# Optimization experiments

Measured on AMD Instinct MI355X. Metric: run time of the kernel, lower is better.

Reference implementation:

```python
import jax, jax.numpy as jnp
import numpy as np
from jax import lax

B, V, E = 8, 1024, 32          # batch, nodes, raw node-embedding dim
F, H = 64, 4                   # node_encoding, num_heads
HID = 64                       # encoder/decoder hidden size
LAYERS = 2                     # graph_layers
FLOW_ITERS = 10
BIG = 1e9
COST_C = 1.0                   # quadratic cost: c*x^2, inv_derivative(y)=y/(2c)
DEG_P = 16.0 / V               # ~16 avg out-degree


def setup_inputs() -> dict:
    key = jax.random.key(0)
    ks = jax.random.split(key, 24)
    demands = jax.random.normal(ks[0], (B, V, 1), jnp.float32)
    demands = demands - jnp.mean(demands, axis=1, keepdims=True)  # balanced supply/demand
    node_embeddings = jax.random.normal(ks[1], (V, E), jnp.float32)
    adj = (jax.random.uniform(ks[2], (V, V)) < DEG_P).astype(jnp.float32)
    adj = jnp.maximum(adj, jnp.eye(V, dtype=jnp.float32))  # ensure nonempty rows
    s = 0.05
    p = lambda k, shp: jax.random.normal(k, shp, jnp.float32) * s
    return {
        'demands': demands, 'node_embeddings': node_embeddings, 'adj': adj,
        'enc_w1': p(ks[3], (E + 1, HID)), 'enc_b1': jnp.zeros((HID,), jnp.float32),
        'enc_w2': p(ks[4], (HID, F)),     'enc_b2': jnp.zeros((F,), jnp.float32),
        'gat_w':  p(ks[5], (H, F, F)),
        'gat_a1': p(ks[6], (H, F)), 'gat_a2': p(ks[7], (H, F)),
        'gate_w': p(ks[8], (F, F)), 'gate_u': p(ks[9], (F, F)),
        'gate_b': jnp.zeros((F,), jnp.float32),
        'dec_w1': p(ks[10], (F, HID)), 'dec_b1': jnp.zeros((HID,), jnp.float32),
        'dec_w2': p(ks[11], (HID, V)), 'dec_b2': jnp.zeros((V,), jnp.float32),
        'dual_w1': p(ks[12], (F, HID)), 'dual_b1': jnp.zeros((HID,), jnp.float32),
        'dual_w2': p(ks[13], (HID, 1)), 'dual_b2': jnp.zeros((1,), jnp.float32),
    }


def _forward(demands, node_embeddings, adj,
             enc_w1, enc_b1, enc_w2, enc_b2,
             gat_w, gat_a1, gat_a2,
             gate_w, gate_u, gate_b,
             dec_w1, dec_b1, dec_w2, dec_b2,
             dual_w1, dual_b1, dual_w2, dual_b2):
    node_bias = -BIG * (1.0 - adj)                     # [V, V]
    # ---- encoder MLP (relu hidden) ----
    x = jnp.broadcast_to(node_embeddings[None], (B, V, E))
    x = jnp.concatenate([x, demands], axis=2)          # [B, V, E+1]
    enc = jax.nn.relu(x @ enc_w1 + enc_b1) @ enc_w2 + enc_b2   # [B, V, F]
    enc = jax.nn.relu(enc)
    # ---- GAT + gate, shared weights across graph_layers ----
    for _ in range(LAYERS):
        t = jnp.einsum('bvf,hfg->bhvg', enc, gat_w)            # [B, H, V, F]
        s_self = jnp.einsum('bhvg,hg->bhv', t, gat_a1)
        s_nbr = jnp.einsum('bhvg,hg->bhv', t, gat_a2)
        logits = jax.nn.leaky_relu(s_self[..., :, None] + s_nbr[..., None, :], 0.2)
        coefs = jax.nn.softmax(logits + node_bias[None, None], axis=-1)  # [B,H,V,V]
        heads = jnp.einsum('bhvw,bhwg->bhvg', coefs, t)
        nxt = jax.nn.relu(jnp.mean(heads, axis=1))             # [B, V, F]
        z = jax.nn.sigmoid(nxt @ gate_w + enc @ gate_u + gate_b)
        enc = z * nxt + (1.0 - z) * enc
    # ---- decoder -> masked softmax flow weights ----
    pred = (enc @ dec_w1 + dec_b1) @ dec_w2 + dec_b2           # [B, V, V] (linear MLP)
    pred = jnp.square(pred)
    flow_weights = jax.nn.softmax(pred + node_bias[None], axis=-1)
    # ---- iterative min-cost-flow solve ----
    def flow_step(flow, _):
        inflow = jnp.sum(flow, axis=1)[:, :, None]             # [B, V, 1]
        return flow_weights * jax.nn.relu(inflow - demands), None
    flow, _ = lax.scan(flow_step, jnp.zeros_like(flow_weights), None, length=FLOW_ITERS)[0], None
    flow = lax.scan(flow_step, jnp.zeros_like(flow_weights), None, length=FLOW_ITERS)[0]
    flow_cost = jnp.sum(COST_C * jnp.square(flow), axis=(1, 2))  # [B]
    # ---- dual variables / dual cost ----
    dv = (enc @ dual_w1 + dual_b1) @ dual_w2 + dual_b2         # [B, V, 1]
    dual_diff = dv - jnp.swapaxes(dv, 1, 2)                    # [B, V, V]
    dual_flows = adj[None] * jax.nn.relu(dual_diff / (2.0 * COST_C))
    dual_flow_cost = COST_C * jnp.square(dual_flows) - dual_diff * dual_flows
    dual_demand = jnp.sum(dv * demands, axis=(1, 2))
    dual_cost = jnp.sum(dual_flow_cost, axis=(1, 2)) - dual_demand
    loss = jnp.mean(flow_cost - dual_cost)
    return loss


def reference(demands, node_embeddings, adj,
              enc_w1, enc_b1, enc_w2, enc_b2,
              gat_w, gat_a1, gat_a2,
              gate_w, gate_u, gate_b,
              dec_w1, dec_b1, dec_w2, dec_b2,
              dual_w1, dual_b1, dual_w2, dual_b2):
    return _forward(demands, node_embeddings, adj,
                    enc_w1, enc_b1, enc_w2, enc_b2,
                    gat_w, gat_a1, gat_a2,
                    gate_w, gate_u, gate_b,
                    dec_w1, dec_b1, dec_w2, dec_b2,
                    dual_w1, dual_b1, dual_w2, dual_b2)
```

## Files before the change

### kernel.cpp

```cpp
#include <hip/hip_runtime.h>
#include <math.h>

#define B 8
#define V 1024
#define E 32
#define H 4
#define HIDN 64
#define CAP 64
#define MAXNNZ 20480
#define SE (MAXNNZ / V)
#define ZBLK 128


__device__ __forceinline__ float wave_sum(float v) {
  for (int o = 32; o > 0; o >>= 1) v += __shfl_xor(v, o);
  return v;
}
__device__ __forceinline__ float wave_max(float v) {
  for (int o = 32; o > 0; o >>= 1) v = fmaxf(v, __shfl_xor(v, o));
  return v;
}

__global__ void zero_wa_kernel(int* __restrict__ deg_in, const float* __restrict__ gat_w,
                               const float* __restrict__ a1, const float* __restrict__ a2,
                               float* __restrict__ wa1, float* __restrict__ wa2) {
  if (blockIdx.x < 4) {
    deg_in[blockIdx.x * 256 + threadIdx.x] = 0;
  } else {
    int h = threadIdx.x >> 6, f = threadIdx.x & 63;
    float s1 = 0.f, s2 = 0.f;
    const float* W = gat_w + h * 4096 + f * 64;
    for (int g = 0; g < 64; ++g) {
      float w = W[g];
      s1 += w * a1[h * 64 + g];
      s2 += w * a2[h * 64 + g];
    }
    wa1[h * 64 + f] = s1;
    wa2[h * 64 + f] = s2;
  }
}

#define ENV 8
__global__ void setup_kernel(const float* __restrict__ adj, const float* __restrict__ demands,
                             const float* __restrict__ emb,
                             const float* __restrict__ ew1, const float* __restrict__ eb1,
                             const float* __restrict__ ew2, const float* __restrict__ eb2,
                             const float* __restrict__ dec_w2,
                             const float* __restrict__ wa1, const float* __restrict__ wa2,
                             int* __restrict__ nbr, int* __restrict__ deg,
                             int* __restrict__ deg_in, float* __restrict__ enc,
                             float* __restrict__ ss, float* __restrict__ sn,
                             float* __restrict__ w2t, float* __restrict__ fwe,
                             unsigned int* __restrict__ meta) {
  int blk = blockIdx.x;
  int j = threadIdx.x;
  if (blk < V) {
    int v = blk;
    int base = 0;
    for (int c = 0; c < V; c += 64) {
      float a = adj[v * V + c + j];
      unsigned long long m = __ballot(a > 0.5f);
      int pos = __popcll(m & ((1ull << j) - 1ull));
      if (a > 0.5f && base + pos < CAP) {
        nbr[v * CAP + base + pos] = c + j;
        atomicAdd(&deg_in[c + j], 1);
      }
      base += __popcll(m);
    }
    if (j == 0) deg[v] = (base < CAP) ? base : CAP;
  } else if (blk < 2 * V) {
    int eb = blk - V;
    int b = eb & 7;
    int v0 = (eb >> 3) * ENV;
    int bv0 = b * V + v0;
    __shared__ float xs[ENV][E + 1];
    __shared__ float hs[ENV][64];
#pragma unroll
    for (int n = 0; n < ENV; ++n) {
      if (j < E) xs[n][j] = emb[(v0 + n) * E + j];
      else if (j == E) xs[n][E] = demands[b * V + v0 + n];
    }
    __syncthreads();
    float h[ENV];
#pragma unroll
    for (int n = 0; n < ENV; ++n) h[n] = eb1[j];
    for (int i = 0; i < E + 1; ++i) {
      float wv = ew1[i * 64 + j];
#pragma unroll
      for (int n = 0; n < ENV; ++n) h[n] += xs[n][i] * wv;
    }
#pragma unroll
    for (int n = 0; n < ENV; ++n) hs[n][j] = fmaxf(h[n], 0.f);
    __syncthreads();
    float o[ENV];
#pragma unroll
    for (int n = 0; n < ENV; ++n) o[n] = eb2[j];
    for (int i = 0; i < 64; ++i) {
      float wv = ew2[i * 64 + j];
#pragma unroll
      for (int n = 0; n < ENV; ++n) o[n] += hs[n][i] * wv;
    }
#pragma unroll
    for (int n = 0; n < ENV; ++n) {
      o[n] = fmaxf(o[n], 0.f);
      enc[(bv0 + n) * 64 + j] = o[n];
    }
#pragma unroll
    for (int n = 0; n < ENV; ++n) {
#pragma unroll
      for (int hh = 0; hh < H; ++hh) {
        float v1 = wave_sum(o[n] * wa1[hh * 64 + j]);
        float v2 = wave_sum(o[n] * wa2[hh * 64 + j]);
        if (j == 0) {
          ss[(b * H + hh) * V + v0 + n] = v1;
          sn[(b * H + hh) * V + v0 + n] = v2;
        }
      }
    }
  } else if (blk < 3 * V) {
    int w = blk - 2 * V;
    w2t[w * 64 + j] = dec_w2[j * V + w];
  } else {
    int idx = (blk - 3 * V) * 64 + j;
    for (int i = idx; i < B * MAXNNZ; i += ZBLK * 64) fwe[i] = 0.f;
    for (int i = idx; i < MAXNNZ; i += ZBLK * 64) meta[i] = 0u;
  }
}

__global__ void scan_kernel(const int* __restrict__ deg_in, int* __restrict__ in_off) {
  int lane = threadIdx.x;
  int vals[16];
  int tot = 0;
#pragma unroll
  for (int i = 0; i < 16; ++i) {
    vals[i] = tot;
    tot += deg_in[lane * 16 + i];
  }
  int run = tot;
  for (int o = 1; o < 64; o <<= 1) {
    int u = __shfl_up(run, o);
    if (lane >= o) run += u;
  }
  int excl = run - tot;
#pragma unroll
  for (int i = 0; i < 16; ++i) in_off[lane * 16 + i] = excl + vals[i];
  if (lane == 63) in_off[V] = excl + tot;
}

__global__ void csc_fill(const int* __restrict__ nbr, const int* __restrict__ deg,
                         int* __restrict__ deg_in, const int* __restrict__ in_off,
                         int* __restrict__ csc_pos) {
  int v = blockIdx.x, k = threadIdx.x;
  if (k < deg[v]) {
    int w = nbr[v * CAP + k];
    int old = atomicSub(&deg_in[w], 1);
    csc_pos[v * CAP + k] = in_off[w] + old - 1;
  }
}

#define GNV 8
__global__ __launch_bounds__(256) void gat2_kernel(
    const float* __restrict__ enc_in, const float* __restrict__ ss_in,
    const float* __restrict__ sn_in, const int* __restrict__ nbr,
    const int* __restrict__ deg, const float* __restrict__ gat_w,
    const float* __restrict__ gate_w, const float* __restrict__ gate_u,
    const float* __restrict__ gate_b, const float* __restrict__ wa1,
    const float* __restrict__ wa2, float* __restrict__ enc_out,
    float* __restrict__ ss_out, float* __restrict__ sn_out, int write_s) {
  int b = blockIdx.x & 7;
  int v0 = (blockIdx.x >> 3) * GNV;
  int tid = threadIdx.x;
  int wid = tid >> 6, lane = tid & 63;
  __shared__ float agg[GNV][H][64];
  __shared__ float gpart[GNV][4][64];
  __shared__ float nxts[GNV][64];
  __shared__ float encs[GNV][64];
  const float* eb = enc_in + (size_t)b * V * 64;
  for (int i = tid; i < GNV * 64; i += 256) encs[i >> 6][i & 63] = eb[v0 * 64 + i];
  for (int n = wid; n < GNV; n += 4) {
    int v = v0 + n;
    int dvv = deg[v];
    int wk = (lane < dvv) ? nbr[v * CAP + lane] : 0;
    float c[H];
#pragma unroll
    for (int h = 0; h < H; ++h) {
      float x = ss_in[(b * H + h) * V + v] + sn_in[(b * H + h) * V + wk];
      x = (x > 0.f) ? x : 0.2f * x;
      if (lane >= dvv) x = -1e30f;
      float m = wave_max(x);
      float e = (lane < dvv) ? __expf(x - m) : 0.f;
      float s = wave_sum(e);
      c[h] = e / s;
    }
    float a0 = 0.f, a1v = 0.f, a2v = 0.f, a3v = 0.f;
    for (int k = 0; k < dvv; ++k) {
      int w = __shfl(wk, k);
      float ev = eb[w * 64 + lane];
      a0 += __shfl(c[0], k) * ev;
      a1v += __shfl(c[1], k) * ev;
      a2v += __shfl(c[2], k) * ev;
      a3v += __shfl(c[3], k) * ev;
    }
    agg[n][0][lane] = a0;
    agg[n][1][lane] = a1v;
    agg[n][2][lane] = a2v;
    agg[n][3][lane] = a3v;
  }
  __syncthreads();
  {
    const float* W = gat_w + wid * 4096;
    float hv[GNV];
#pragma unroll
    for (int n = 0; n < GNV; ++n) hv[n] = 0.f;
    for (int f = 0; f < 64; ++f) {
      float wf = W[f * 64 + lane];
#pragma unroll
      for (int n = 0; n < GNV; ++n) hv[n] += agg[n][wid][f] * wf;
    }
#pragma unroll
    for (int n = 0; n < GNV; ++n) gpart[n][wid][lane] = hv[n];
  }
  __syncthreads();
  for (int i = tid; i < GNV * 64; i += 256) {
    int n = i >> 6, g = i & 63;
    float s4 = gpart[n][0][g] + gpart[n][1][g] + gpart[n][2][g] + gpart[n][3][g];
    nxts[n][g] = fmaxf(0.25f * s4, 0.f);
  }
  __syncthreads();
  {
    float part[GNV];
#pragma unroll
    for (int n = 0; n < GNV; ++n) part[n] = 0.f;
    for (int f = wid * 16; f < wid * 16 + 16; ++f) {
      float gw = gate_w[f * 64 + lane], gu = gate_u[f * 64 + lane];
#pragma unroll
      for (int n = 0; n < GNV; ++n) part[n] += nxts[n][f] * gw + encs[n][f] * gu;
    }
    __syncthreads();
#pragma unroll
    for (int n = 0; n < GNV; ++n) gpart[n][wid][lane] = part[n];
  }
  __syncthreads();
  for (int i = tid; i < GNV * 64; i += 256) {
    int n = i >> 6, g = i & 63;
    float zs = gpart[n][0][g] + gpart[n][1][g] + gpart[n][2][g] + gpart[n][3][g] + gate_b[g];
    float z = 1.f / (1.f + __expf(-zs));
    float out = z * nxts[n][g] + (1.f - z) * encs[n][g];
    encs[n][g] = out;
    enc_out[((size_t)b * V + v0 + n) * 64 + g] = out;
  }
  if (write_s) {
    __syncthreads();
    float w1v = wa1[wid * 64 + lane], w2v = wa2[wid * 64 + lane];
#pragma unroll
    for (int n = 0; n < GNV; ++n) {
      float e = encs[n][lane];
      float ssv = wave_sum(e * w1v);
      float snv = wave_sum(e * w2v);
      if (lane == 0) {
        ss_out[(b * H + wid) * V + v0 + n] = ssv;
        sn_out[(b * H + wid) * V + v0 + n] = snv;
      }
    }
  }
}

#define DNV 8
__global__ void dec_dual_kernel(const float* __restrict__ enc, const float* __restrict__ dw1,
                                const float* __restrict__ db1, const float* __restrict__ uw1,
                                const float* __restrict__ ub1, const float* __restrict__ uw2,
                                const float* __restrict__ ub2, float* __restrict__ hid,
                                float* __restrict__ dv) {
  int b = blockIdx.x & 7;
  int v0 = (blockIdx.x >> 3) * DNV;
  int bv0 = b * V + v0;
  int j = threadIdx.x;
  __shared__ float es[DNV][64];
#pragma unroll
  for (int n = 0; n < DNV; ++n) es[n][j] = enc[(bv0 + n) * 64 + j];
  __syncthreads();
  float hj[DNV], uj[DNV];
#pragma unroll
  for (int n = 0; n < DNV; ++n) { hj[n] = db1[j]; uj[n] = ub1[j]; }
  for (int f = 0; f < 64; ++f) {
    float a = dw1[f * 64 + j], c = uw1[f * 64 + j];
#pragma unroll
    for (int n = 0; n < DNV; ++n) {
      hj[n] += es[n][f] * a;
      uj[n] += es[n][f] * c;
    }
  }
  float w2v = uw2[j];
#pragma unroll
  for (int n = 0; n < DNV; ++n) {
    hid[(bv0 + n) * 64 + j] = hj[n];
    float s = wave_sum(uj[n] * w2v);
    if (j == 0) dv[bv0 + n] = s + ub2[0];
  }
}

__global__ void fw_kernel(const float* __restrict__ hid, const float* __restrict__ w2t,
                          const float* __restrict__ b2, const int* __restrict__ nbr,
                          const int* __restrict__ deg, const int* __restrict__ csc_pos,
                          float* __restrict__ fwe, unsigned int* __restrict__ meta,
                          float* __restrict__ rssq) {
  int b = blockIdx.x & 7;
  int v = blockIdx.x >> 3;
  int bv = b * V + v;
  int k = threadIdx.x;
  __shared__ float hs[64];
  hs[k] = hid[bv * 64 + k];
  __syncthreads();
  int dvv = deg[v];
  int w = (k < dvv) ? nbr[v * CAP + k] : 0;
  const float4* wrow = (const float4*)(w2t + w * 64);
  const float4* hv4 = (const float4*)hs;
  float d = 0.f;
#pragma unroll
  for (int f = 0; f < 16; ++f) {
    float4 wv = wrow[f];
    float4 hv = hv4[f];
    d += hv.x * wv.x + hv.y * wv.y + hv.z * wv.z + hv.w * wv.w;
  }
  d += b2[w];
  float pp = d * d;
  float myp = (k < dvv) ? pp : -1e30f;
  float m = wave_max(myp);
  float e = (k < dvv) ? __expf(myp - m) : 0.f;
  float s = wave_sum(e);
  float coef = e / s;
  if (k < dvv) {
    int idx = csc_pos[v * CAP + k];
    fwe[(size_t)b * MAXNNZ + idx] = coef;
    meta[idx] = (unsigned)v | ((unsigned)w << 16);
  }
  float r = wave_sum(coef * coef);
  if (k == 0) rssq[bv] = r;
}

__global__ __launch_bounds__(1024) void flow_dual_kernel(
    const float* __restrict__ fwe, const unsigned int* __restrict__ meta,
    const float* __restrict__ rssq, const float* __restrict__ dv,
    const float* __restrict__ demands, const int* __restrict__ nbr_out,
    const int* __restrict__ deg_out, float* __restrict__ partial) {
  int b = blockIdx.x;
  int v = threadIdx.x;
  __shared__ float o[V], infl[V], dvs[V];
  __shared__ float red[16];
  float dem = demands[b * V + v];
  dvs[v] = dv[b * V + v];
  o[v] = fmaxf(-dem, 0.f);
  infl[v] = 0.f;
  const float4* fp = (const float4*)(fwe + (size_t)b * MAXNNZ + v * SE);
  const uint4* mp = (const uint4*)(meta + v * SE);
  float fr[SE];
  unsigned mr[SE];
#pragma unroll
  for (int i = 0; i < SE / 4; ++i) {
    float4 f4 = fp[i];
    uint4 m4 = mp[i];
    fr[4 * i + 0] = f4.x; fr[4 * i + 1] = f4.y; fr[4 * i + 2] = f4.z; fr[4 * i + 3] = f4.w;
    mr[4 * i + 0] = m4.x; mr[4 * i + 1] = m4.y; mr[4 * i + 2] = m4.z; mr[4 * i + 3] = m4.w;
  }
  __syncthreads();
  for (int it = 0; it < 9; ++it) {
    float acc = 0.f;
    int pdst = -1;
#pragma unroll
    for (int i = 0; i < SE; ++i) {
      int src = mr[i] & 0xFFFF;
      int dst = mr[i] >> 16;
      if (dst != pdst) {
        if (acc != 0.f) atomicAdd(&infl[pdst], acc);
        acc = 0.f;
        pdst = dst;
      }
      acc += fr[i] * o[src];
    }
    if (acc != 0.f) atomicAdd(&infl[pdst], acc);
    __syncthreads();
    float nv = fmaxf(infl[v] - dem, 0.f);
    o[v] = nv;
    infl[v] = 0.f;
    __syncthreads();
  }
  float o10 = o[v];
  float local = o10 * o10 * rssq[b * V + v];
  float dvv = dvs[v];
  int dout = deg_out[v];
  float acc = 0.f;
  for (int k = 0; k < dout; ++k) {
    float diff = dvv - dvs[nbr_out[v * CAP + k]];
    if (diff > 0.f) acc += diff * diff;
  }
  local += 0.25f * acc + dvv * dem;
  local = wave_sum(local);
  if ((v & 63) == 0) red[v >> 6] = local;
  __syncthreads();
  if (v < 16) {
    float r = red[v];
    for (int o2 = 8; o2 > 0; o2 >>= 1) r += __shfl_xor(r, o2, 16);
    if (v == 0) partial[b] = r;
  }
}

__global__ void final_kernel(const float* __restrict__ partial, float* __restrict__ out) {
  if (threadIdx.x == 0) {
    float s = 0.f;
    for (int b = 0; b < B; ++b) s += partial[b];
    out[0] = s * (1.0f / B);
  }
}

extern "C" void kernel_launch(void* const* d_in, const int* in_sizes, int n_in,
                              void* d_out, int out_size, void* d_ws, size_t ws_size,
                              hipStream_t stream) {
  const float* demands = (const float*)d_in[0];
  const float* emb     = (const float*)d_in[1];
  const float* adj     = (const float*)d_in[2];
  const float* enc_w1  = (const float*)d_in[3];
  const float* enc_b1  = (const float*)d_in[4];
  const float* enc_w2  = (const float*)d_in[5];
  const float* enc_b2  = (const float*)d_in[6];
  const float* gat_w   = (const float*)d_in[7];
  const float* gat_a1  = (const float*)d_in[8];
  const float* gat_a2  = (const float*)d_in[9];
  const float* gate_w  = (const float*)d_in[10];
  const float* gate_u  = (const float*)d_in[11];
  const float* gate_b  = (const float*)d_in[12];
  const float* dec_w1  = (const float*)d_in[13];
  const float* dec_b1  = (const float*)d_in[14];
  const float* dec_w2  = (const float*)d_in[15];
  const float* dec_b2  = (const float*)d_in[16];
  const float* dual_w1 = (const float*)d_in[17];
  const float* dual_b1 = (const float*)d_in[18];
  const float* dual_w2 = (const float*)d_in[19];
  const float* dual_b2 = (const float*)d_in[20];

  char* p = (char*)d_ws;
  auto alloc = [&](size_t n) { void* r = (void*)p; p += (n + 255) & ~(size_t)255; return r; };
  int* nbr_out   = (int*)alloc((size_t)V * CAP * 4);
  int* deg_out   = (int*)alloc((size_t)V * 4);
  int* deg_in    = (int*)alloc((size_t)V * 4);
  int* in_off    = (int*)alloc((size_t)(V + 1) * 4);
  int* csc_pos   = (int*)alloc((size_t)V * CAP * 4);
  float* fwe     = (float*)alloc((size_t)B * MAXNNZ * 4);
  unsigned int* meta = (unsigned int*)alloc((size_t)MAXNNZ * 4);
  float* w2t     = (float*)alloc((size_t)HIDN * V * 4);
  float* wa1     = (float*)alloc((size_t)H * 64 * 4);
  float* wa2     = (float*)alloc((size_t)H * 64 * 4);
  float* encA    = (float*)alloc((size_t)B * V * 64 * 4);
  float* encB    = (float*)alloc((size_t)B * V * 64 * 4);
  float* ssA     = (float*)alloc((size_t)B * H * V * 4);
  float* snA     = (float*)alloc((size_t)B * H * V * 4);
  float* ssB     = (float*)alloc((size_t)B * H * V * 4);
  float* snB     = (float*)alloc((size_t)B * H * V * 4);
  float* hid     = (float*)alloc((size_t)B * V * 64 * 4);
  float* dv      = (float*)alloc((size_t)B * V * 4);
  float* rssq    = (float*)alloc((size_t)B * V * 4);
  float* partial = (float*)alloc((size_t)B * 4);

  zero_wa_kernel<<<5, 256, 0, stream>>>(deg_in, gat_w, gat_a1, gat_a2, wa1, wa2);
  setup_kernel<<<3 * V + ZBLK, 64, 0, stream>>>(
      adj, demands, emb, enc_w1, enc_b1, enc_w2, enc_b2, dec_w2, wa1, wa2,
      nbr_out, deg_out, deg_in, encA, ssA, snA, w2t, fwe, meta);
  scan_kernel<<<1, 64, 0, stream>>>(deg_in, in_off);
  csc_fill<<<V, 64, 0, stream>>>(nbr_out, deg_out, deg_in, in_off, csc_pos);
  gat2_kernel<<<B * V / GNV, 256, 0, stream>>>(encA, ssA, snA, nbr_out, deg_out, gat_w,
                                               gate_w, gate_u, gate_b, wa1, wa2,
                                               encB, ssB, snB, 1);
  gat2_kernel<<<B * V / GNV, 256, 0, stream>>>(encB, ssB, snB, nbr_out, deg_out, gat_w,
                                               gate_w, gate_u, gate_b, wa1, wa2,
                                               encA, ssA, snA, 0);
  dec_dual_kernel<<<B * V / DNV, 64, 0, stream>>>(encA, dec_w1, dec_b1, dual_w1, dual_b1,
                                                  dual_w2, dual_b2, hid, dv);
  fw_kernel<<<B * V, 64, 0, stream>>>(hid, w2t, dec_b2, nbr_out, deg_out, csc_pos,
                                      fwe, meta, rssq);
  flow_dual_kernel<<<B, 1024, 0, stream>>>(fwe, meta, rssq, dv, demands, nbr_out, deg_out,
                                           partial);
  final_kernel<<<1, 64, 0, stream>>>(partial, (float*)d_out);
}
```

Baseline: 150.9 us.

## Merge pipeline into fewer uniform-grid phase kernels with fused scan and final reduction

Regroups the original ten launches into an init kernel, four fixed-size 512x256 phase kernels and the flow kernel. The CSC scan and fill now run inside the first GAT phase, using an atomic slot counter in place of the decrementing degree counter. The decoder/dual stage is fused with the edge softmax so the hidden activations stay in shared memory. The final mean is done by the last flow block through an atomic done counter. The aim is to cut launch overhead and intermediate global traffic, at the cost of changed block shapes, per-block serial work and an atomic handshake.

```diff
diff --git a/kernel.cpp b/kernel.cpp
--- a/kernel.cpp
+++ b/kernel.cpp
@@ -5,11 +5,11 @@
 #define V 1024
 #define E 32
 #define H 4
-#define HIDN 64
 #define CAP 64
 #define MAXNNZ 20480
 #define SE (MAXNNZ / V)
-#define ZBLK 128
+#define NBLK 512
+#define NTHR 256
 
 
 __device__ __forceinline__ float wave_sum(float v) {
@@ -21,13 +21,29 @@
   return v;
 }
 
-__global__ void zero_wa_kernel(int* __restrict__ deg_in, const float* __restrict__ gat_w,
-                               const float* __restrict__ a1, const float* __restrict__ a2,
-                               float* __restrict__ wa1, float* __restrict__ wa2) {
-  if (blockIdx.x < 4) {
-    deg_in[blockIdx.x * 256 + threadIdx.x] = 0;
+struct Params {
+  const float *adj, *demands, *emb;
+  const float *ew1, *eb1, *ew2, *eb2, *dec_w2;
+  const float *gat_w, *ga1, *ga2, *gate_w, *gate_u, *gate_b;
+  const float *dw1, *db1, *uw1, *ub1, *uw2, *ub2, *dec_b2;
+  int *nbr, *deg, *deg_in, *slot_cur, *csc_pos;
+  float *fwe;
+  unsigned *meta;
+  float *w2t, *wa1, *wa2, *encA, *encB, *ssA, *snA, *ssB, *snB, *dvp, *rssq;
+};
+
+__global__ void init_kernel(int* __restrict__ deg_in, int* __restrict__ slot_cur,
+                            unsigned* __restrict__ done, const float* __restrict__ gat_w,
+                            const float* __restrict__ a1, const float* __restrict__ a2,
+                            float* __restrict__ wa1, float* __restrict__ wa2) {
+  int blk = blockIdx.x, tid = threadIdx.x;
+  if (blk < 4) {
+    deg_in[blk * 256 + tid] = 0;
+  } else if (blk < 8) {
+    slot_cur[(blk - 4) * 256 + tid] = 0;
   } else {
-    int h = threadIdx.x >> 6, f = threadIdx.x & 63;
+    if (tid == 0) *done = 0u;
+    int h = tid >> 6, f = tid & 63;
     float s1 = 0.f, s2 = 0.f;
     const float* W = gat_w + h * 4096 + f * 64;
     for (int g = 0; g < 64; ++g) {
@@ -40,309 +56,303 @@
   }
 }
 
-#define ENV 8
-__global__ void setup_kernel(const float* __restrict__ adj, const float* __restrict__ demands,
-                             const float* __restrict__ emb,
-                             const float* __restrict__ ew1, const float* __restrict__ eb1,
-                             const float* __restrict__ ew2, const float* __restrict__ eb2,
-                             const float* __restrict__ dec_w2,
-                             const float* __restrict__ wa1, const float* __restrict__ wa2,
-                             int* __restrict__ nbr, int* __restrict__ deg,
-                             int* __restrict__ deg_in, float* __restrict__ enc,
-                             float* __restrict__ ss, float* __restrict__ sn,
-                             float* __restrict__ w2t, float* __restrict__ fwe,
-                             unsigned int* __restrict__ meta) {
-  int blk = blockIdx.x;
-  int j = threadIdx.x;
-  if (blk < V) {
-    int v = blk;
-    int base = 0;
-    for (int c = 0; c < V; c += 64) {
-      float a = adj[v * V + c + j];
-      unsigned long long m = __ballot(a > 0.5f);
-      int pos = __popcll(m & ((1ull << j) - 1ull));
-      if (a > 0.5f && base + pos < CAP) {
-        nbr[v * CAP + base + pos] = c + j;
-        atomicAdd(&deg_in[c + j], 1);
-      }
-      base += __popcll(m);
-    }
-    if (j == 0) deg[v] = (base < CAP) ? base : CAP;
-  } else if (blk < 2 * V) {
-    int eb = blk - V;
-    int b = eb & 7;
-    int v0 = (eb >> 3) * ENV;
-    int bv0 = b * V + v0;
-    __shared__ float xs[ENV][E + 1];
-    __shared__ float hs[ENV][64];
-#pragma unroll
-    for (int n = 0; n < ENV; ++n) {
-      if (j < E) xs[n][j] = emb[(v0 + n) * E + j];
-      else if (j == E) xs[n][E] = demands[b * V + v0 + n];
-    }
-    __syncthreads();
-    float h[ENV];
-#pragma unroll
-    for (int n = 0; n < ENV; ++n) h[n] = eb1[j];
-    for (int i = 0; i < E + 1; ++i) {
-      float wv = ew1[i * 64 + j];
-#pragma unroll
-      for (int n = 0; n < ENV; ++n) h[n] += xs[n][i] * wv;
-    }
-#pragma unroll
-    for (int n = 0; n < ENV; ++n) hs[n][j] = fmaxf(h[n], 0.f);
-    __syncthreads();
-    float o[ENV];
-#pragma unroll
-    for (int n = 0; n < ENV; ++n) o[n] = eb2[j];
-    for (int i = 0; i < 64; ++i) {
-      float wv = ew2[i * 64 + j];
-#pragma unroll
-      for (int n = 0; n < ENV; ++n) o[n] += hs[n][i] * wv;
-    }
-#pragma unroll
-    for (int n = 0; n < ENV; ++n) {
-      o[n] = fmaxf(o[n], 0.f);
-      enc[(bv0 + n) * 64 + j] = o[n];
-    }
-#pragma unroll
-    for (int n = 0; n < ENV; ++n) {
-#pragma unroll
-      for (int hh = 0; hh < H; ++hh) {
-        float v1 = wave_sum(o[n] * wa1[hh * 64 + j]);
-        float v2 = wave_sum(o[n] * wa2[hh * 64 + j]);
-        if (j == 0) {
-          ss[(b * H + hh) * V + v0 + n] = v1;
-          sn[(b * H + hh) * V + v0 + n] = v2;
+__global__ __launch_bounds__(NTHR) void p0_kernel(Params p) {
+  __shared__ float arena[3104];
+  int blk = blockIdx.x, tid = threadIdx.x, wid = tid >> 6, lane = tid & 63;
+  if (blk < 128) {
+    for (int rr = 0; rr < 2; ++rr) {
+      int v = blk * 8 + wid * 2 + rr;
+      int base = 0;
+      for (int c = 0; c < V; c += 64) {
+        float a = p.adj[(size_t)v * V + c + lane];
+        unsigned long long m = __ballot(a > 0.5f);
+        int pos = __popcll(m & ((1ull << lane) - 1ull));
+        if (a > 0.5f && base + pos < CAP) {
+          p.nbr[v * CAP + base + pos] = c + lane;
+          atomicAdd(&p.deg_in[c + lane], 1);
         }
-      }
-    }
-  } else if (blk < 3 * V) {
-    int w = blk - 2 * V;
-    w2t[w * 64 + j] = dec_w2[j * V + w];
+        base += __popcll(m);
+      }
+      if (lane == 0) p.deg[v] = (base < CAP) ? base : CAP;
+    }
+  } else if (blk < 256) {
+    int bb = blk - 128;
+    float wa1r[4], wa2r[4];
+#pragma unroll
+    for (int h = 0; h < 4; ++h) {
+      wa1r[h] = p.wa1[h * 64 + lane];
+      wa2r[h] = p.wa2[h * 64 + lane];
+    }
+    float* xs = arena + wid * 264;
+    float* hsw = arena + 1056 + wid * 512;
+    for (int uu = 0; uu < 2; ++uu) {
+      int unit = (bb >> 3) * 64 + (wid * 2 + uu) * 8 + (bb & 7);
+      int b = unit & 7, v0 = (unit >> 3) * 8, bv0 = b * V + v0;
+#pragma unroll
+      for (int n = 0; n < 8; ++n) {
+        if (lane < E) xs[n * 33 + lane] = p.emb[(v0 + n) * E + lane];
+        else if (lane == E) xs[n * 33 + E] = p.demands[b * V + v0 + n];
+      }
+      float h8[8];
+#pragma unroll
+      for (int n = 0; n < 8; ++n) h8[n] = p.eb1[lane];
+      for (int i = 0; i < E + 1; ++i) {
+        float wv = p.ew1[i * 64 + lane];
+#pragma unroll
+        for (int n = 0; n < 8; ++n) h8[n] += xs[n * 33 + i] * wv;
+      }
+#pragma unroll
+      for (int n = 0; n < 8; ++n) hsw[n * 64 + lane] = fmaxf(h8[n], 0.f);
+      float o8[8];
+#pragma unroll
+      for (int n = 0; n < 8; ++n) o8[n] = p.eb2[lane];
+      for (int i = 0; i < 64; ++i) {
+        float wv = p.ew2[i * 64 + lane];
+#pragma unroll
+        for (int n = 0; n < 8; ++n) o8[n] += hsw[n * 64 + i] * wv;
+      }
+#pragma unroll
+      for (int n = 0; n < 8; ++n) {
+        o8[n] = fmaxf(o8[n], 0.f);
+        p.encA[(size_t)(bv0 + n) * 64 + lane] = o8[n];
+      }
+#pragma unroll
+      for (int n = 0; n < 8; ++n) {
+#pragma unroll
+        for (int hh = 0; hh < 4; ++hh) {
+          float v1 = wave_sum(o8[n] * wa1r[hh]);
+          float v2 = wave_sum(o8[n] * wa2r[hh]);
+          if (lane == 0) {
+            p.ssA[(b * 4 + hh) * V + v0 + n] = v1;
+            p.snA[(b * 4 + hh) * V + v0 + n] = v2;
+          }
+        }
+      }
+    }
+  } else if (blk < 384) {
+    for (int rr = 0; rr < 2; ++rr) {
+      int col = (blk - 256) * 8 + wid * 2 + rr;
+      p.w2t[col * 64 + lane] = p.dec_w2[(size_t)lane * V + col];
+    }
   } else {
-    int idx = (blk - 3 * V) * 64 + j;
-    for (int i = idx; i < B * MAXNNZ; i += ZBLK * 64) fwe[i] = 0.f;
-    for (int i = idx; i < MAXNNZ; i += ZBLK * 64) meta[i] = 0u;
-  }
-}
-
-__global__ void scan_kernel(const int* __restrict__ deg_in, int* __restrict__ in_off) {
-  int lane = threadIdx.x;
-  int vals[16];
-  int tot = 0;
-#pragma unroll
-  for (int i = 0; i < 16; ++i) {
-    vals[i] = tot;
-    tot += deg_in[lane * 16 + i];
-  }
-  int run = tot;
-  for (int o = 1; o < 64; o <<= 1) {
-    int u = __shfl_up(run, o);
-    if (lane >= o) run += u;
-  }
-  int excl = run - tot;
-#pragma unroll
-  for (int i = 0; i < 16; ++i) in_off[lane * 16 + i] = excl + vals[i];
-  if (lane == 63) in_off[V] = excl + tot;
-}
-
-__global__ void csc_fill(const int* __restrict__ nbr, const int* __restrict__ deg,
-                         int* __restrict__ deg_in, const int* __restrict__ in_off,
-                         int* __restrict__ csc_pos) {
-  int v = blockIdx.x, k = threadIdx.x;
-  if (k < deg[v]) {
-    int w = nbr[v * CAP + k];
-    int old = atomicSub(&deg_in[w], 1);
-    csc_pos[v * CAP + k] = in_off[w] + old - 1;
-  }
-}
-
-#define GNV 8
-__global__ __launch_bounds__(256) void gat2_kernel(
-    const float* __restrict__ enc_in, const float* __restrict__ ss_in,
-    const float* __restrict__ sn_in, const int* __restrict__ nbr,
-    const int* __restrict__ deg, const float* __restrict__ gat_w,
-    const float* __restrict__ gate_w, const float* __restrict__ gate_u,
-    const float* __restrict__ gate_b, const float* __restrict__ wa1,
-    const float* __restrict__ wa2, float* __restrict__ enc_out,
-    float* __restrict__ ss_out, float* __restrict__ sn_out, int write_s) {
-  int b = blockIdx.x & 7;
-  int v0 = (blockIdx.x >> 3) * GNV;
-  int tid = threadIdx.x;
-  int wid = tid >> 6, lane = tid & 63;
-  __shared__ float agg[GNV][H][64];
-  __shared__ float gpart[GNV][4][64];
-  __shared__ float nxts[GNV][64];
-  __shared__ float encs[GNV][64];
+    int idx = (blk - 384) * 256 + tid;
+    for (int i = idx; i < B * MAXNNZ; i += 128 * 256) p.fwe[i] = 0.f;
+    for (int i = idx; i < MAXNNZ; i += 128 * 256) p.meta[i] = 0u;
+  }
+}
+
+__device__ static void gat2_pass(const Params& p, const float* __restrict__ enc_in,
+                                 const float* __restrict__ ss_in, const float* __restrict__ sn_in,
+                                 float* __restrict__ enc_out, float* __restrict__ ss_out,
+                                 float* __restrict__ sn_out, int write_s, int unit,
+                                 float* arena) {
+  int tid = threadIdx.x, wid = tid >> 6, lane = tid & 63;
+  int b = unit & 7, v0 = (unit >> 3) * 8;
+  float* agg = arena;
+  float* gpart = arena + 2048;
+  float* nxts = arena + 4096;
+  float* encs = arena + 4608;
   const float* eb = enc_in + (size_t)b * V * 64;
-  for (int i = tid; i < GNV * 64; i += 256) encs[i >> 6][i & 63] = eb[v0 * 64 + i];
-  for (int n = wid; n < GNV; n += 4) {
+  __syncthreads();
+  for (int i = tid; i < 512; i += 256) encs[i] = eb[v0 * 64 + i];
+  for (int n = wid; n < 8; n += 4) {
     int v = v0 + n;
-    int dvv = deg[v];
-    int wk = (lane < dvv) ? nbr[v * CAP + lane] : 0;
-    float c[H];
-#pragma unroll
-    for (int h = 0; h < H; ++h) {
-      float x = ss_in[(b * H + h) * V + v] + sn_in[(b * H + h) * V + wk];
+    int dvv = p.deg[v];
+    int wk = (lane < dvv) ? p.nbr[v * CAP + lane] : 0;
+    float cc[4];
+#pragma unroll
+    for (int h = 0; h < 4; ++h) {
+      float x = ss_in[(b * 4 + h) * V + v] + sn_in[(b * 4 + h) * V + wk];
       x = (x > 0.f) ? x : 0.2f * x;
       if (lane >= dvv) x = -1e30f;
       float m = wave_max(x);
       float e = (lane < dvv) ? __expf(x - m) : 0.f;
       float s = wave_sum(e);
-      c[h] = e / s;
-    }
-    float a0 = 0.f, a1v = 0.f, a2v = 0.f, a3v = 0.f;
+      cc[h] = e / s;
+    }
+    float a0 = 0.f, a1 = 0.f, a2 = 0.f, a3 = 0.f;
     for (int k = 0; k < dvv; ++k) {
       int w = __shfl(wk, k);
       float ev = eb[w * 64 + lane];
-      a0 += __shfl(c[0], k) * ev;
-      a1v += __shfl(c[1], k) * ev;
-      a2v += __shfl(c[2], k) * ev;
-      a3v += __shfl(c[3], k) * ev;
-    }
-    agg[n][0][lane] = a0;
-    agg[n][1][lane] = a1v;
-    agg[n][2][lane] = a2v;
-    agg[n][3][lane] = a3v;
+      a0 += __shfl(cc[0], k) * ev;
+      a1 += __shfl(cc[1], k) * ev;
+      a2 += __shfl(cc[2], k) * ev;
+      a3 += __shfl(cc[3], k) * ev;
+    }
+    agg[(n * 4 + 0) * 64 + lane] = a0;
+    agg[(n * 4 + 1) * 64 + lane] = a1;
+    agg[(n * 4 + 2) * 64 + lane] = a2;
+    agg[(n * 4 + 3) * 64 + lane] = a3;
   }
   __syncthreads();
   {
-    const float* W = gat_w + wid * 4096;
-    float hv[GNV];
-#pragma unroll
-    for (int n = 0; n < GNV; ++n) hv[n] = 0.f;
+    const float* W = p.gat_w + wid * 4096;
+    float hv[8];
+#pragma unroll
+    for (int n = 0; n < 8; ++n) hv[n] = 0.f;
     for (int f = 0; f < 64; ++f) {
       float wf = W[f * 64 + lane];
 #pragma unroll
-      for (int n = 0; n < GNV; ++n) hv[n] += agg[n][wid][f] * wf;
-    }
-#pragma unroll
-    for (int n = 0; n < GNV; ++n) gpart[n][wid][lane] = hv[n];
-  }
-  __syncthreads();
-  for (int i = tid; i < GNV * 64; i += 256) {
+      for (int n = 0; n < 8; ++n) hv[n] += agg[(n * 4 + wid) * 64 + f] * wf;
+    }
+#pragma unroll
+    for (int n = 0; n < 8; ++n) gpart[(n * 4 + wid) * 64 + lane] = hv[n];
+  }
+  __syncthreads();
+  for (int i = tid; i < 512; i += 256) {
     int n = i >> 6, g = i & 63;
-    float s4 = gpart[n][0][g] + gpart[n][1][g] + gpart[n][2][g] + gpart[n][3][g];
-    nxts[n][g] = fmaxf(0.25f * s4, 0.f);
+    float s4 = gpart[(n * 4) * 64 + g] + gpart[(n * 4 + 1) * 64 + g] +
+               gpart[(n * 4 + 2) * 64 + g] + gpart[(n * 4 + 3) * 64 + g];
+    nxts[i] = fmaxf(0.25f * s4, 0.f);
   }
   __syncthreads();
   {
-    float part[GNV];
-#pragma unroll
-    for (int n = 0; n < GNV; ++n) part[n] = 0.f;
+    float part[8];
+#pragma unroll
+    for (int n = 0; n < 8; ++n) part[n] = 0.f;
     for (int f = wid * 16; f < wid * 16 + 16; ++f) {
-      float gw = gate_w[f * 64 + lane], gu = gate_u[f * 64 + lane];
-#pragma unroll
-      for (int n = 0; n < GNV; ++n) part[n] += nxts[n][f] * gw + encs[n][f] * gu;
+      float gw = p.gate_w[f * 64 + lane], gu = p.gate_u[f * 64 + lane];
+#pragma unroll
+      for (int n = 0; n < 8; ++n) part[n] += nxts[n * 64 + f] * gw + encs[n * 64 + f] * gu;
     }
     __syncthreads();
 #pragma unroll
-    for (int n = 0; n < GNV; ++n) gpart[n][wid][lane] = part[n];
-  }
-  __syncthreads();
-  for (int i = tid; i < GNV * 64; i += 256) {
+    for (int n = 0; n < 8; ++n) gpart[(n * 4 + wid) * 64 + lane] = part[n];
+  }
+  __syncthreads();
+  for (int i = tid; i < 512; i += 256) {
     int n = i >> 6, g = i & 63;
-    float zs = gpart[n][0][g] + gpart[n][1][g] + gpart[n][2][g] + gpart[n][3][g] + gate_b[g];
+    float zs = gpart[(n * 4) * 64 + g] + gpart[(n * 4 + 1) * 64 + g] +
+               gpart[(n * 4 + 2) * 64 + g] + gpart[(n * 4 + 3) * 64 + g] + p.gate_b[g];
     float z = 1.f / (1.f + __expf(-zs));
-    float out = z * nxts[n][g] + (1.f - z) * encs[n][g];
-    encs[n][g] = out;
+    float out = z * nxts[i] + (1.f - z) * encs[i];
+    encs[i] = out;
     enc_out[((size_t)b * V + v0 + n) * 64 + g] = out;
   }
   if (write_s) {
     __syncthreads();
-    float w1v = wa1[wid * 64 + lane], w2v = wa2[wid * 64 + lane];
-#pragma unroll
-    for (int n = 0; n < GNV; ++n) {
-      float e = encs[n][lane];
-      float ssv = wave_sum(e * w1v);
-      float snv = wave_sum(e * w2v);
+    float w1v = p.wa1[wid * 64 + lane], w2v = p.wa2[wid * 64 + lane];
+#pragma unroll
+    for (int n = 0; n < 8; ++n) {
+      float e2 = encs[n * 64 + lane];
+      float ssv = wave_sum(e2 * w1v);
+      float snv = wave_sum(e2 * w2v);
       if (lane == 0) {
-        ss_out[(b * H + wid) * V + v0 + n] = ssv;
-        sn_out[(b * H + wid) * V + v0 + n] = snv;
-      }
-    }
-  }
-}
-
-#define DNV 8
-__global__ void dec_dual_kernel(const float* __restrict__ enc, const float* __restrict__ dw1,
-                                const float* __restrict__ db1, const float* __restrict__ uw1,
-                                const float* __restrict__ ub1, const float* __restrict__ uw2,
-                                const float* __restrict__ ub2, float* __restrict__ hid,
-                                float* __restrict__ dv) {
-  int b = blockIdx.x & 7;
-  int v0 = (blockIdx.x >> 3) * DNV;
+        ss_out[(b * 4 + wid) * V + v0 + n] = ssv;
+        sn_out[(b * 4 + wid) * V + v0 + n] = snv;
+      }
+    }
+  }
+}
+
+__global__ __launch_bounds__(NTHR) void p1_kernel(Params p) {
+  __shared__ float arena[6144];
+  int blk = blockIdx.x, tid = threadIdx.x, wid = tid >> 6, lane = tid & 63;
+  for (int ps = 0; ps < 2; ++ps) {
+    int unit = ((blk >> 3) * 2 + ps) * 8 + (blk & 7);
+    gat2_pass(p, p.encA, p.ssA, p.snA, p.encB, p.ssB, p.snB, 1, unit, arena);
+  }
+  __syncthreads();
+  int* ioff = (int*)(arena + 5120);
+  if (tid < 64) {
+    int vals[16];
+    int tot = 0;
+#pragma unroll
+    for (int i = 0; i < 16; ++i) {
+      vals[i] = tot;
+      tot += p.deg_in[tid * 16 + i];
+    }
+    int run = tot;
+    for (int o = 1; o < 64; o <<= 1) {
+      int u = __shfl_up(run, o);
+      if (lane >= o) run += u;
+    }
+    int excl = run - tot;
+#pragma unroll
+    for (int i = 0; i < 16; ++i) ioff[tid * 16 + i] = excl + vals[i];
+  }
+  __syncthreads();
+  if (wid < 2) {
+    int v = blk * 2 + wid;
+    if (lane < p.deg[v]) {
+      int w = p.nbr[v * CAP + lane];
+      p.csc_pos[v * CAP + lane] = ioff[w] + atomicAdd(&p.slot_cur[w], 1);
+    }
+  }
+}
+
+__global__ __launch_bounds__(NTHR) void p2_kernel(Params p) {
+  __shared__ float arena[6144];
+  int blk = blockIdx.x;
+  for (int ps = 0; ps < 2; ++ps) {
+    int unit = ((blk >> 3) * 2 + ps) * 8 + (blk & 7);
+    gat2_pass(p, p.encB, p.ssB, p.snB, p.encA, p.ssA, p.snA, 0, unit, arena);
+  }
+}
+
+__global__ __launch_bounds__(NTHR) void p3_kernel(Params p) {
+  __shared__ float arena[2048];
+  int blk = blockIdx.x, tid = threadIdx.x, wid = tid >> 6, lane = tid & 63;
+  int b = blk & 7, v0 = (blk >> 3) * 16 + wid * 4;
   int bv0 = b * V + v0;
-  int j = threadIdx.x;
-  __shared__ float es[DNV][64];
-#pragma unroll
-  for (int n = 0; n < DNV; ++n) es[n][j] = enc[(bv0 + n) * 64 + j];
-  __syncthreads();
-  float hj[DNV], uj[DNV];
-#pragma unroll
-  for (int n = 0; n < DNV; ++n) { hj[n] = db1[j]; uj[n] = ub1[j]; }
+  float* es = arena + wid * 256;
+  float* hsd = arena + 1024 + wid * 256;
+#pragma unroll
+  for (int n = 0; n < 4; ++n) es[n * 64 + lane] = p.encA[(size_t)(bv0 + n) * 64 + lane];
+  float hj[4], uj[4];
+#pragma unroll
+  for (int n = 0; n < 4; ++n) { hj[n] = p.db1[lane]; uj[n] = p.ub1[lane]; }
   for (int f = 0; f < 64; ++f) {
-    float a = dw1[f * 64 + j], c = uw1[f * 64 + j];
-#pragma unroll
-    for (int n = 0; n < DNV; ++n) {
-      hj[n] += es[n][f] * a;
-      uj[n] += es[n][f] * c;
-    }
-  }
-  float w2v = uw2[j];
-#pragma unroll
-  for (int n = 0; n < DNV; ++n) {
-    hid[(bv0 + n) * 64 + j] = hj[n];
+    float a = p.dw1[f * 64 + lane], c = p.uw1[f * 64 + lane];
+#pragma unroll
+    for (int n = 0; n < 4; ++n) {
+      hj[n] += es[n * 64 + f] * a;
+      uj[n] += es[n * 64 + f] * c;
+    }
+  }
+  float w2v = p.uw2[lane];
+#pragma unroll
+  for (int n = 0; n < 4; ++n) {
+    hsd[n * 64 + lane] = hj[n];
     float s = wave_sum(uj[n] * w2v);
-    if (j == 0) dv[bv0 + n] = s + ub2[0];
-  }
-}
-
-__global__ void fw_kernel(const float* __restrict__ hid, const float* __restrict__ w2t,
-                          const float* __restrict__ b2, const int* __restrict__ nbr,
-                          const int* __restrict__ deg, const int* __restrict__ csc_pos,
-                          float* __restrict__ fwe, unsigned int* __restrict__ meta,
-                          float* __restrict__ rssq) {
-  int b = blockIdx.x & 7;
-  int v = blockIdx.x >> 3;
-  int bv = b * V + v;
-  int k = threadIdx.x;
-  __shared__ float hs[64];
-  hs[k] = hid[bv * 64 + k];
-  __syncthreads();
-  int dvv = deg[v];
-  int w = (k < dvv) ? nbr[v * CAP + k] : 0;
-  const float4* wrow = (const float4*)(w2t + w * 64);
-  const float4* hv4 = (const float4*)hs;
-  float d = 0.f;
-#pragma unroll
-  for (int f = 0; f < 16; ++f) {
-    float4 wv = wrow[f];
-    float4 hv = hv4[f];
-    d += hv.x * wv.x + hv.y * wv.y + hv.z * wv.z + hv.w * wv.w;
-  }
-  d += b2[w];
-  float pp = d * d;
-  float myp = (k < dvv) ? pp : -1e30f;
-  float m = wave_max(myp);
-  float e = (k < dvv) ? __expf(myp - m) : 0.f;
-  float s = wave_sum(e);
-  float coef = e / s;
-  if (k < dvv) {
-    int idx = csc_pos[v * CAP + k];
-    fwe[(size_t)b * MAXNNZ + idx] = coef;
-    meta[idx] = (unsigned)v | ((unsigned)w << 16);
-  }
-  float r = wave_sum(coef * coef);
-  if (k == 0) rssq[bv] = r;
+    if (lane == 0) p.dvp[bv0 + n] = s + p.ub2[0];
+  }
+  for (int n = 0; n < 4; ++n) {
+    int v = v0 + n;
+    int dvv = p.deg[v];
+    int w = (lane < dvv) ? p.nbr[v * CAP + lane] : 0;
+    const float4* wrow = (const float4*)(p.w2t + w * 64);
+    const float4* hv4 = (const float4*)(hsd + n * 64);
+    float d = 0.f;
+#pragma unroll
+    for (int f = 0; f < 16; ++f) {
+      float4 wv = wrow[f];
+      float4 hv = hv4[f];
+      d += hv.x * wv.x + hv.y * wv.y + hv.z * wv.z + hv.w * wv.w;
+    }
+    d += p.dec_b2[w];
+    float pp = d * d;
+    float myp = (lane < dvv) ? pp : -1e30f;
+    float m = wave_max(myp);
+    float e = (lane < dvv) ? __expf(myp - m) : 0.f;
+    float s = wave_sum(e);
+    float coef = e / s;
+    if (lane < dvv) {
+      int idx = p.csc_pos[v * CAP + lane];
+      p.fwe[(size_t)b * MAXNNZ + idx] = coef;
+      p.meta[idx] = (unsigned)v | ((unsigned)w << 16);
+    }
+    float r = wave_sum(coef * coef);
+    if (lane == 0) p.rssq[bv0 + n] = r;
+  }
 }
 
 __global__ __launch_bounds__(1024) void flow_dual_kernel(
-    const float* __restrict__ fwe, const unsigned int* __restrict__ meta,
+    const float* __restrict__ fwe, const unsigned* __restrict__ meta,
     const float* __restrict__ rssq, const float* __restrict__ dv,
     const float* __restrict__ demands, const int* __restrict__ nbr_out,
-    const int* __restrict__ deg_out, float* __restrict__ partial) {
+    const int* __restrict__ deg_out, float* __restrict__ partial,
+    unsigned* __restrict__ done, float* __restrict__ out) {
   int b = blockIdx.x;
   int v = threadIdx.x;
   __shared__ float o[V], infl[V], dvs[V];
@@ -400,83 +410,67 @@
   if (v < 16) {
     float r = red[v];
     for (int o2 = 8; o2 > 0; o2 >>= 1) r += __shfl_xor(r, o2, 16);
-    if (v == 0) partial[b] = r;
-  }
-}
-
-__global__ void final_kernel(const float* __restrict__ partial, float* __restrict__ out) {
-  if (threadIdx.x == 0) {
-    float s = 0.f;
-    for (int b = 0; b < B; ++b) s += partial[b];
-    out[0] = s * (1.0f / B);
+    if (v == 0) {
+      __hip_atomic_store(&partial[b], r, __ATOMIC_RELEASE, __HIP_MEMORY_SCOPE_AGENT);
+      unsigned old = __hip_atomic_fetch_add(done, 1u, __ATOMIC_ACQ_REL, __HIP_MEMORY_SCOPE_AGENT);
+      if (old == B - 1) {
+        float s = 0.f;
+        for (int i = 0; i < B; ++i)
+          s += __hip_atomic_load(&partial[i], __ATOMIC_ACQUIRE, __HIP_MEMORY_SCOPE_AGENT);
+        out[0] = s * (1.0f / B);
+      }
+    }
   }
 }
 
 extern "C" void kernel_launch(void* const* d_in, const int* in_sizes, int n_in,
                               void* d_out, int out_size, void* d_ws, size_t ws_size,
                               hipStream_t stream) {
-  const float* demands = (const float*)d_in[0];
-  const float* emb     = (const float*)d_in[1];
-  const float* adj     = (const float*)d_in[2];
-  const float* enc_w1  = (const float*)d_in[3];
-  const float* enc_b1  = (const float*)d_in[4];
-  const float* enc_w2  = (const float*)d_in[5];
-  const float* enc_b2  = (const float*)d_in[6];
-  const float* gat_w   = (const float*)d_in[7];
-  const float* gat_a1  = (const float*)d_in[8];
-  const float* gat_a2  = (const float*)d_in[9];
-  const float* gate_w  = (const float*)d_in[10];
-  const float* gate_u  = (const float*)d_in[11];
-  const float* gate_b  = (const float*)d_in[12];
-  const float* dec_w1  = (const float*)d_in[13];
-  const float* dec_b1  = (const float*)d_in[14];
-  const float* dec_w2  = (const float*)d_in[15];
-  const float* dec_b2  = (const float*)d_in[16];
-  const float* dual_w1 = (const float*)d_in[17];
-  const float* dual_b1 = (const float*)d_in[18];
-  const float* dual_w2 = (const float*)d_in[19];
-  const float* dual_b2 = (const float*)d_in[20];
-
-  char* p = (char*)d_ws;
+  Params P;
+  P.adj     = (const float*)d_in[2];
+  P.demands = (const float*)d_in[0];
+  P.emb     = (const float*)d_in[1];
+  P.ew1 = (const float*)d_in[3];  P.eb1 = (const float*)d_in[4];
+  P.ew2 = (const float*)d_in[5];  P.eb2 = (const float*)d_in[6];
+  P.gat_w = (const float*)d_in[7];
+  P.ga1 = (const float*)d_in[8];  P.ga2 = (const float*)d_in[9];
+  P.gate_w = (const float*)d_in[10]; P.gate_u = (const float*)d_in[11];
+  P.gate_b = (const float*)d_in[12];
+  P.dw1 = (const float*)d_in[13]; P.db1 = (const float*)d_in[14];
+  P.dec_w2 = (const float*)d_in[15]; P.dec_b2 = (const float*)d_in[16];
+  P.uw1 = (const float*)d_in[17]; P.ub1 = (const float*)d_in[18];
+  P.uw2 = (const float*)d_in[19]; P.ub2 = (const float*)d_in[20];
+
+  char* pz = (char*)d_ws;
+  P.deg_in   = (int*)pz;
+  P.slot_cur = (int*)(pz + 4096);
+  unsigned* done = (unsigned*)(pz + 8192);
+  char* p = pz + 8448;
   auto alloc = [&](size_t n) { void* r = (void*)p; p += (n + 255) & ~(size_t)255; return r; };
-  int* nbr_out   = (int*)alloc((size_t)V * CAP * 4);
-  int* deg_out   = (int*)alloc((size_t)V * 4);
-  int* deg_in    = (int*)alloc((size_t)V * 4);
-  int* in_off    = (int*)alloc((size_t)(V + 1) * 4);
-  int* csc_pos   = (int*)alloc((size_t)V * CAP * 4);
-  float* fwe     = (float*)alloc((size_t)B * MAXNNZ * 4);
-  unsigned int* meta = (unsigned int*)alloc((size_t)MAXNNZ * 4);
-  float* w2t     = (float*)alloc((size_t)HIDN * V * 4);
-  float* wa1     = (float*)alloc((size_t)H * 64 * 4);
-  float* wa2     = (float*)alloc((size_t)H * 64 * 4);
-  float* encA    = (float*)alloc((size_t)B * V * 64 * 4);
-  float* encB    = (float*)alloc((size_t)B * V * 64 * 4);
-  float* ssA     = (float*)alloc((size_t)B * H * V * 4);
-  float* snA     = (float*)alloc((size_t)B * H * V * 4);
-  float* ssB     = (float*)alloc((size_t)B * H * V * 4);
-  float* snB     = (float*)alloc((size_t)B * H * V * 4);
-  float* hid     = (float*)alloc((size_t)B * V * 64 * 4);
-  float* dv      = (float*)alloc((size_t)B * V * 4);
-  float* rssq    = (float*)alloc((size_t)B * V * 4);
+  P.nbr     = (int*)alloc((size_t)V * CAP * 4);
+  P.deg     = (int*)alloc((size_t)V * 4);
+  P.csc_pos = (int*)alloc((size_t)V * CAP * 4);
+  P.fwe     = (float*)alloc((size_t)B * MAXNNZ * 4);
+  P.meta    = (unsigned*)alloc((size_t)MAXNNZ * 4);
+  P.w2t     = (float*)alloc((size_t)64 * V * 4);
+  P.wa1     = (float*)alloc((size_t)H * 64 * 4);
+  P.wa2     = (float*)alloc((size_t)H * 64 * 4);
+  P.encA    = (float*)alloc((size_t)B * V * 64 * 4);
+  P.encB    = (float*)alloc((size_t)B * V * 64 * 4);
+  P.ssA     = (float*)alloc((size_t)B * H * V * 4);
+  P.snA     = (float*)alloc((size_t)B * H * V * 4);
+  P.ssB     = (float*)alloc((size_t)B * H * V * 4);
+  P.snB     = (float*)alloc((size_t)B * H * V * 4);
+  P.dvp     = (float*)alloc((size_t)B * V * 4);
+  P.rssq    = (float*)alloc((size_t)B * V * 4);
   float* partial = (float*)alloc((size_t)B * 4);
 
-  zero_wa_kernel<<<5, 256, 0, stream>>>(deg_in, gat_w, gat_a1, gat_a2, wa1, wa2);
-  setup_kernel<<<3 * V + ZBLK, 64, 0, stream>>>(
-      adj, demands, emb, enc_w1, enc_b1, enc_w2, enc_b2, dec_w2, wa1, wa2,
-      nbr_out, deg_out, deg_in, encA, ssA, snA, w2t, fwe, meta);
-  scan_kernel<<<1, 64, 0, stream>>>(deg_in, in_off);
-  csc_fill<<<V, 64, 0, stream>>>(nbr_out, deg_out, deg_in, in_off, csc_pos);
-  gat2_kernel<<<B * V / GNV, 256, 0, stream>>>(encA, ssA, snA, nbr_out, deg_out, gat_w,
-                                               gate_w, gate_u, gate_b, wa1, wa2,
-                                               encB, ssB, snB, 1);
-  gat2_kernel<<<B * V / GNV, 256, 0, stream>>>(encB, ssB, snB, nbr_out, deg_out, gat_w,
-                                               gate_w, gate_u, gate_b, wa1, wa2,
-                                               encA, ssA, snA, 0);
-  dec_dual_kernel<<<B * V / DNV, 64, 0, stream>>>(encA, dec_w1, dec_b1, dual_w1, dual_b1,
-                                                  dual_w2, dual_b2, hid, dv);
-  fw_kernel<<<B * V, 64, 0, stream>>>(hid, w2t, dec_b2, nbr_out, deg_out, csc_pos,
-                                      fwe, meta, rssq);
-  flow_dual_kernel<<<B, 1024, 0, stream>>>(fwe, meta, rssq, dv, demands, nbr_out, deg_out,
-                                           partial);
-  final_kernel<<<1, 64, 0, stream>>>(partial, (float*)d_out);
-}
+  init_kernel<<<9, 256, 0, stream>>>(P.deg_in, P.slot_cur, done, P.gat_w, P.ga1, P.ga2,
+                                     P.wa1, P.wa2);
+  p0_kernel<<<NBLK, NTHR, 0, stream>>>(P);
+  p1_kernel<<<NBLK, NTHR, 0, stream>>>(P);
+  p2_kernel<<<NBLK, NTHR, 0, stream>>>(P);
+  p3_kernel<<<NBLK, NTHR, 0, stream>>>(P);
+  flow_dual_kernel<<<B, 1024, 0, stream>>>(P.fwe, P.meta, P.rssq, P.dvp, P.demands,
+                                           P.nbr, P.deg, partial, done, (float*)d_out);
+}
```

Result: slower. 230.1 us (+52.4%).
